# Performance work log

Hardware: AMD Instinct MI355X
Metric: run time of the kernel (lower is better)

The kernel has to match this reference:

```python
import jax, jax.numpy as jnp
import numpy as np

D_MODEL = 1024
N_HEADS = 16
HEAD_DIM = D_MODEL // N_HEADS
FFN_DIM = 4096
N_EXPERTS = 8
CAP_FRAC = 0.25          # moe_eval_capacity_token_fraction (eval mode)
MOE_TOKEN_DROPOUT = 0.2  # eval: expert output scaled by (1 - p)
LN_EPS = 1e-5
B, S = 4, 512


def setup_inputs():
    key = jax.random.key(0)
    ks = jax.random.split(key, 20)
    def w(k, shape, scale=0.02):
        return jax.random.normal(k, shape, jnp.float32) * scale
    return {
        "x": jax.random.normal(ks[0], (B, S, D_MODEL), jnp.float32),
        "wq": w(ks[1], (D_MODEL, D_MODEL)), "bq": w(ks[2], (D_MODEL,)),
        "wk": w(ks[3], (D_MODEL, D_MODEL)), "bk": w(ks[4], (D_MODEL,)),
        "wv": w(ks[5], (D_MODEL, D_MODEL)), "bv": w(ks[6], (D_MODEL,)),
        "wo": w(ks[7], (D_MODEL, D_MODEL)), "bo": w(ks[8], (D_MODEL,)),
        "ln1_g": 1.0 + w(ks[9], (D_MODEL,)), "ln1_b": w(ks[10], (D_MODEL,)),
        "ln2_g": 1.0 + w(ks[11], (D_MODEL,)), "ln2_b": w(ks[12], (D_MODEL,)),
        "wr": w(ks[13], (D_MODEL, N_EXPERTS)),
        "w1": w(ks[14], (N_EXPERTS, D_MODEL, FFN_DIM)), "b1": w(ks[15], (N_EXPERTS, FFN_DIM)),
        "w2": w(ks[16], (N_EXPERTS, FFN_DIM, D_MODEL)), "b2": w(ks[17], (N_EXPERTS, D_MODEL)),
    }


def _layer_norm(x, g, b):
    mu = x.mean(-1, keepdims=True)
    var = ((x - mu) ** 2).mean(-1, keepdims=True)
    return (x - mu) * jax.lax.rsqrt(var + LN_EPS) * g + b


def _self_attention(x, wq, bq, wk, bk, wv, bv, wo, bo):
    b, s, d = x.shape
    q = ((x @ wq + bq) * (HEAD_DIM ** -0.5)).reshape(b, s, N_HEADS, HEAD_DIM)
    k = (x @ wk + bk).reshape(b, s, N_HEADS, HEAD_DIM)
    v = (x @ wv + bv).reshape(b, s, N_HEADS, HEAD_DIM)
    scores = jnp.einsum('bqhd,bkhd->bhqk', q, k)
    p = jax.nn.softmax(scores, axis=-1)
    o = jnp.einsum('bhqk,bkhd->bqhd', p, v).reshape(b, s, d)
    return o @ wo + bo


def _moe_ffn(x, wr, w1, b1, w2, b2):
    # x: [T, D]. NLLB-MoE top-2 router with capacity dropping (eval mode,
    # second_expert_policy='all', normalize_router_prob_before_dropping=False).
    T, D = x.shape
    C = int(np.ceil(CAP_FRAC * T))  # static expert capacity
    logits = x @ wr                                    # [T, E] router dtype fp32
    probs = jax.nn.softmax(logits, axis=-1)
    top1 = jnp.argmax(probs, axis=-1)                  # [T]
    m1 = jax.nn.one_hot(top1, N_EXPERTS, dtype=x.dtype)
    top2 = jnp.argmax(jnp.where(m1 > 0, -jnp.inf, logits), axis=-1)
    m2 = jax.nn.one_hot(top2, N_EXPERTS, dtype=x.dtype)
    loc1 = jnp.cumsum(m1, axis=0) - 1.0                # slot within expert
    loc2 = jnp.cumsum(m2, axis=0) - 1.0 + m1.sum(0, keepdims=True)
    m1 = m1 * (loc1 < C)                               # capacity dropping
    m2 = m2 * (loc2 < C)
    t1 = (probs * m1).sum(-1)
    t2 = (probs * m2).sum(-1)
    denom = jnp.maximum(t1 + t2, jnp.finfo(x.dtype).eps)
    t1, t2 = t1 / denom, t2 / denom
    tok = jnp.arange(T)
    s1 = loc1[tok, top1].astype(jnp.int32)
    s2 = loc2[tok, top2].astype(jnp.int32)
    v1 = m1[tok, top1] > 0
    v2 = m2[tok, top2] > 0
    s1 = jnp.where(v1, s1, C)  # out-of-range slot -> dropped by scatter
    s2 = jnp.where(v2, s2, C)
    # dispatch tokens to capacity buffers [E, C, D] (slots are unique)
    buf = jnp.zeros((N_EXPERTS, C, D), x.dtype)
    buf = buf.at[top1, s1].set(x, mode='drop')
    buf = buf.at[top2, s2].set(x, mode='drop')
    # grouped expert FFN (relu), eval-mode moe_token_dropout scaling
    h = jax.nn.relu(jnp.einsum('ecd,edf->ecf', buf, w1) + b1[:, None, :])
    y = (jnp.einsum('ecf,efd->ecd', h, w2) + b2[:, None, :]) * (1.0 - MOE_TOKEN_DROPOUT)
    # combine with normalized top-2 gates (dropped tokens get gate 0)
    y1 = y[top1, jnp.minimum(s1, C - 1)]
    y2 = y[top2, jnp.minimum(s2, C - 1)]
    g1 = t1 * v1
    g2 = t2 * v2
    return g1[:, None] * y1 + g2[:, None] * y2


def reference(x, wq, bq, wk, bk, wv, bv, wo, bo, ln1_g, ln1_b, ln2_g, ln2_b, wr, w1, b1, w2, b2):
    # Pre-LN self-attention block
    h = _layer_norm(x, ln1_g, ln1_b)
    h = _self_attention(h, wq, bq, wk, bk, wv, bv, wo, bo)
    x = x + h
    # Pre-LN sparse MoE FFN block
    h = _layer_norm(x, ln2_g, ln2_b)
    b, s, d = h.shape
    moe = _moe_ffn(h.reshape(b * s, d), wr, w1, b1, w2, b2).reshape(b, s, d)
    return x + moe
```

## Files before the change

### kernel.cpp

```cpp
#include <hip/hip_runtime.h>
#include <hip/hip_bf16.h>
#include <stdint.h>

#define T_TOK 2048
#define DM 1024
#define NHEAD 16
#define HDIM 64
#define SEQ 512
#define NEXP 8
#define FFN 4096
#define CAP 512
#define LN_EPSV 1e-5f
#define ROUTER_EPS 1.1920929e-07f

typedef __bf16 bf16x8 __attribute__((ext_vector_type(8)));
typedef float f32x4 __attribute__((ext_vector_type(4)));

__device__ __forceinline__ void gld_lds16(const __hip_bfloat16* g, __hip_bfloat16* l) {
  __builtin_amdgcn_global_load_lds(
      (const __attribute__((address_space(1))) void*)g,
      (__attribute__((address_space(3))) void*)l, 16, 0, 0);
}

__device__ __forceinline__ void xcd_remap(int& bx, int& by, int& bz) {
  int gx = gridDim.x, gy = gridDim.y, gz = gridDim.z;
  int nwg = gx * gy * gz;
  int lin = (blockIdx.z * gy + blockIdx.y) * gx + blockIdx.x;
  int q = nwg >> 3;
  int lin2 = (lin & 7) * q + (lin >> 3);
  int gxy = gx * gy;
  bz = lin2 / gxy;
  int rem = lin2 - bz * gxy;
  by = rem / gx;
  bx = rem - by * gx;
}

__global__ void transpose_cvt(const float* __restrict__ W, __hip_bfloat16* __restrict__ WT,
                              int R, int Cc) {
  __shared__ float tile[32][33];
  int e = blockIdx.z;
  const float* src = W + (size_t)e * R * Cc;
  __hip_bfloat16* dst = WT + (size_t)e * R * Cc;
  int c0 = blockIdx.x * 32, r0 = blockIdx.y * 32;
  int tx = threadIdx.x, ty = threadIdx.y;
#pragma unroll
  for (int i = 0; i < 4; i++) {
    int r = r0 + ty + i * 8;
    tile[ty + i * 8][tx] = src[(size_t)r * Cc + c0 + tx];
  }
  __syncthreads();
#pragma unroll
  for (int i = 0; i < 4; i++) {
    int c = c0 + ty + i * 8;
    dst[(size_t)c * R + r0 + tx] = __float2bfloat16(tile[tx][ty + i * 8]);
  }
}

__global__ void transpose_cvt_hp(const float* __restrict__ W, __hip_bfloat16* __restrict__ WH,
                                 __hip_bfloat16* __restrict__ WL, int R, int Cc, float scale) {
  __shared__ float tile[32][33];
  int c0 = blockIdx.x * 32, r0 = blockIdx.y * 32;
  int tx = threadIdx.x, ty = threadIdx.y;
#pragma unroll
  for (int i = 0; i < 4; i++) {
    int r = r0 + ty + i * 8;
    tile[ty + i * 8][tx] = W[(size_t)r * Cc + c0 + tx];
  }
  __syncthreads();
#pragma unroll
  for (int i = 0; i < 4; i++) {
    int c = c0 + ty + i * 8;
    float v = tile[tx][ty + i * 8] * scale;
    __hip_bfloat16 h = __float2bfloat16(v);
    WH[(size_t)c * R + r0 + tx] = h;
    WL[(size_t)c * R + r0 + tx] = __float2bfloat16(v - __bfloat162float(h));
  }
}

__global__ __launch_bounds__(256) void pack_bias(const float* __restrict__ bq,
                                                 const float* __restrict__ bk,
                                                 const float* __restrict__ bv,
                                                 float* __restrict__ outp) {
  int t = blockIdx.x * 256 + threadIdx.x;
  if (t < DM) outp[t] = bq[t] * 0.125f;
  else if (t < 2 * DM) outp[t] = bk[t - DM];
  else if (t < 3 * DM) outp[t] = bv[t - 2 * DM];
}

__global__ __launch_bounds__(256) void ln1_hp(const float* __restrict__ x,
                                              const float* __restrict__ g,
                                              const float* __restrict__ bta,
                                              __hip_bfloat16* __restrict__ ohi,
                                              __hip_bfloat16* __restrict__ olo) {
  int row = blockIdx.x, t = threadIdx.x;
  const float4* xr = (const float4*)(x + (size_t)row * DM);
  float4 v = xr[t];
  float s = v.x + v.y + v.z + v.w;
  float ss = v.x * v.x + v.y * v.y + v.z * v.z + v.w * v.w;
  __shared__ float rs[4], rss[4];
  __shared__ float smu, sinv;
  int wid = t >> 6, lane = t & 63;
  for (int off = 32; off; off >>= 1) { s += __shfl_down(s, off); ss += __shfl_down(ss, off); }
  if (!lane) { rs[wid] = s; rss[wid] = ss; }
  __syncthreads();
  if (!t) {
    float S = rs[0] + rs[1] + rs[2] + rs[3], SS = rss[0] + rss[1] + rss[2] + rss[3];
    float mu = S / DM;
    float var = SS / DM - mu * mu;
    smu = mu; sinv = 1.0f / sqrtf(var + LN_EPSV);
  }
  __syncthreads();
  float mu = smu, inv = sinv;
  float4 gv = ((const float4*)g)[t], bv = ((const float4*)bta)[t];
  float n[4];
  n[0] = (v.x - mu) * inv * gv.x + bv.x;
  n[1] = (v.y - mu) * inv * gv.y + bv.y;
  n[2] = (v.z - mu) * inv * gv.z + bv.z;
  n[3] = (v.w - mu) * inv * gv.w + bv.w;
  __hip_bfloat16* hr = ohi + (size_t)row * DM + t * 4;
  __hip_bfloat16* lr = olo + (size_t)row * DM + t * 4;
#pragma unroll
  for (int k = 0; k < 4; k++) {
    __hip_bfloat16 h = __float2bfloat16(n[k]);
    hr[k] = h;
    lr[k] = __float2bfloat16(n[k] - __bfloat162float(h));
  }
}

__global__ __launch_bounds__(256) void cvt_hp(const float* __restrict__ in,
                                              __hip_bfloat16* __restrict__ hi,
                                              __hip_bfloat16* __restrict__ lo) {
  int i = (blockIdx.x * 256 + threadIdx.x) * 4;
  float4 v = *(const float4*)&in[i];
  float n[4] = {v.x, v.y, v.z, v.w};
#pragma unroll
  for (int k = 0; k < 4; k++) {
    __hip_bfloat16 h = __float2bfloat16(n[k]);
    hi[i + k] = h;
    lo[i + k] = __float2bfloat16(n[k] - __bfloat162float(h));
  }
}

template <int BM, int BN, int TM, int TN, bool BT>
__global__ __launch_bounds__(256) void gemm_f32(
    const float* __restrict__ A, const float* __restrict__ B, float* __restrict__ Cc,
    const float* __restrict__ bias, const float* __restrict__ resid,
    int M, int N, int K, int lda, int ldb, int ldc, float scale, int zdiv,
    long long sA1, long long sA2, long long sB1, long long sB2,
    long long sC1, long long sC2) {
  constexpr int BK = 16;
  __shared__ float As[BK][BM + 4];
  __shared__ float Bs[BK][BN + 4];
  int z = blockIdx.z;
  int zq = z / zdiv, zr = z % zdiv;
  A += zq * sA1 + zr * sA2;
  B += zq * sB1 + zr * sB2;
  Cc += zq * sC1 + zr * sC2;
  int tid = threadIdx.x;
  int m0 = blockIdx.y * BM, n0 = blockIdx.x * BN;
  constexpr int NTX = BN / TN;
  int tx = tid % NTX, ty = tid / NTX;
  float acc[TM][TN] = {};
  for (int k0 = 0; k0 < K; k0 += BK) {
    constexpr int ALOADS = BM * BK / (256 * 4);
#pragma unroll
    for (int i = 0; i < ALOADS; i++) {
      int idx = tid + i * 256;
      int m = idx / (BK / 4);
      int kk = (idx % (BK / 4)) * 4;
      float4 va = *(const float4*)&A[(size_t)(m0 + m) * lda + k0 + kk];
      As[kk + 0][m] = va.x; As[kk + 1][m] = va.y; As[kk + 2][m] = va.z; As[kk + 3][m] = va.w;
    }
    constexpr int BLOADS = BK * BN / (256 * 4);
    if (!BT) {
#pragma unroll
      for (int i = 0; i < BLOADS; i++) {
        int idx = tid + i * 256;
        int kk = idx / (BN / 4);
        int n = (idx % (BN / 4)) * 4;
        *(float4*)&Bs[kk][n] = *(const float4*)&B[(size_t)(k0 + kk) * ldb + n0 + n];
      }
    } else {
#pragma unroll
      for (int i = 0; i < BLOADS; i++) {
        int idx = tid + i * 256;
        int n = idx / (BK / 4);
        int kk = (idx % (BK / 4)) * 4;
        float4 vb = *(const float4*)&B[(size_t)(n0 + n) * ldb + k0 + kk];
        Bs[kk + 0][n] = vb.x; Bs[kk + 1][n] = vb.y; Bs[kk + 2][n] = vb.z; Bs[kk + 3][n] = vb.w;
      }
    }
    __syncthreads();
#pragma unroll
    for (int kk = 0; kk < BK; kk++) {
      float ar[TM], br[TN];
#pragma unroll
      for (int i = 0; i < TM; i += 4) *(float4*)&ar[i] = *(const float4*)&As[kk][ty * TM + i];
#pragma unroll
      for (int j = 0; j < TN; j += 4) *(float4*)&br[j] = *(const float4*)&Bs[kk][tx * TN + j];
#pragma unroll
      for (int i = 0; i < TM; i++)
#pragma unroll
        for (int j = 0; j < TN; j++) acc[i][j] += ar[i] * br[j];
    }
    __syncthreads();
  }
#pragma unroll
  for (int i = 0; i < TM; i++) {
    int m = m0 + ty * TM + i;
#pragma unroll
    for (int j = 0; j < TN; j++) {
      int n = n0 + tx * TN + j;
      float v = acc[i][j];
      if (bias) v += bias[n];
      v *= scale;
      if (resid) v += resid[(size_t)m * ldc + n];
      acc[i][j] = v;
    }
#pragma unroll
    for (int j = 0; j < TN; j += 4)
      *(float4*)&Cc[(size_t)m * ldc + n0 + tx * TN + j] = *(float4*)&acc[i][j];
  }
}

__global__ __launch_bounds__(256) void softmax_rows(float* __restrict__ sc) {
  int row = blockIdx.x, t = threadIdx.x;
  float* p = sc + (size_t)row * SEQ;
  float2 v = *(const float2*)&p[t * 2];
  float mx = fmaxf(v.x, v.y);
  __shared__ float r[4];
  __shared__ float bmax, bsum;
  int wid = t >> 6, lane = t & 63;
  for (int off = 32; off; off >>= 1) mx = fmaxf(mx, __shfl_down(mx, off));
  if (!lane) r[wid] = mx;
  __syncthreads();
  if (!t) bmax = fmaxf(fmaxf(r[0], r[1]), fmaxf(r[2], r[3]));
  __syncthreads();
  mx = bmax;
  float e0 = __expf(v.x - mx), e1v = __expf(v.y - mx);
  float s = e0 + e1v;
  for (int off = 32; off; off >>= 1) s += __shfl_down(s, off);
  if (!lane) r[wid] = s;
  __syncthreads();
  if (!t) bsum = r[0] + r[1] + r[2] + r[3];
  __syncthreads();
  float inv = 1.0f / bsum;
  float2 o; o.x = e0 * inv; o.y = e1v * inv;
  *(float2*)&p[t * 2] = o;
}

template <int MODE>
__global__ __launch_bounds__(256) void gemm_hp(
    const __hip_bfloat16* __restrict__ Ahi, const __hip_bfloat16* __restrict__ Alo,
    const __hip_bfloat16* __restrict__ Bhi, const __hip_bfloat16* __restrict__ Blo,
    float* __restrict__ Cc, const float* __restrict__ bias, const float* __restrict__ resid,
    int M, int N, int K, long long sB, long long sC, int biasStride) {
  constexpr int BM = 128, BN = 128, BK = 32;
  __shared__ __align__(16) __hip_bfloat16 AsH[2][BM * BK];
  __shared__ __align__(16) __hip_bfloat16 AsL[2][BM * BK];
  __shared__ __align__(16) __hip_bfloat16 BsH[2][BN * BK];
  __shared__ __align__(16) __hip_bfloat16 BsL[2][BN * BK];
  int bx, by, bz;
  xcd_remap(bx, by, bz);
  int e = bz;
  Bhi += (size_t)e * sB; Blo += (size_t)e * sB;
  size_t czoff = (size_t)e * sC;
  const float* bvec = bias + (size_t)e * biasStride;
  int m0 = by * BM, n0 = bx * BN;
  int tid = threadIdx.x;
  int lane = tid & 63, quad = lane >> 4, l16 = lane & 15, wv = tid >> 6;
  int wm = wv >> 1, wn = wv & 1;
  f32x4 acc[4][4] = {};
  auto STAGE = [&](int buf, int k0) {
#pragma unroll
    for (int i = 0; i < 2; i++) {
      int flat = tid + i * 256;
      int r = flat >> 2, lc = flat & 3;
      int pc = lc ^ ((r >> 1) & 3);
      gld_lds16(Ahi + (size_t)(m0 + r) * K + k0 + pc * 8, &AsH[buf][flat * 8]);
      gld_lds16(Alo + (size_t)(m0 + r) * K + k0 + pc * 8, &AsL[buf][flat * 8]);
      gld_lds16(Bhi + (size_t)(n0 + r) * K + k0 + pc * 8, &BsH[buf][flat * 8]);
      gld_lds16(Blo + (size_t)(n0 + r) * K + k0 + pc * 8, &BsL[buf][flat * 8]);
    }
  };
  STAGE(0, 0);
  __syncthreads();
  int KT = K / BK;
  for (int kt = 0; kt < KT; kt++) {
    int cur = kt & 1;
    if (kt + 1 < KT) STAGE(cur ^ 1, (kt + 1) * BK);
    bf16x8 ah[4], al[4], bh[4], bl[4];
#pragma unroll
    for (int i = 0; i < 4; i++) {
      int r = wm * 64 + i * 16 + l16;
      int pc = quad ^ ((r >> 1) & 3);
      ah[i] = *(const bf16x8*)(&AsH[cur][r * BK + pc * 8]);
      al[i] = *(const bf16x8*)(&AsL[cur][r * BK + pc * 8]);
    }
#pragma unroll
    for (int j = 0; j < 4; j++) {
      int r = wn * 64 + j * 16 + l16;
      int pc = quad ^ ((r >> 1) & 3);
      bh[j] = *(const bf16x8*)(&BsH[cur][r * BK + pc * 8]);
      bl[j] = *(const bf16x8*)(&BsL[cur][r * BK + pc * 8]);
    }
#pragma unroll
    for (int i = 0; i < 4; i++)
#pragma unroll
      for (int j = 0; j < 4; j++) {
        acc[i][j] = __builtin_amdgcn_mfma_f32_16x16x32_bf16(ah[i], bh[j], acc[i][j], 0, 0, 0);
        acc[i][j] = __builtin_amdgcn_mfma_f32_16x16x32_bf16(ah[i], bl[j], acc[i][j], 0, 0, 0);
        acc[i][j] = __builtin_amdgcn_mfma_f32_16x16x32_bf16(al[i], bh[j], acc[i][j], 0, 0, 0);
      }
    __syncthreads();
  }
#pragma unroll
  for (int j = 0; j < 4; j++) {
    int col = n0 + wn * 64 + j * 16 + l16;
    float bb = bvec[col];
#pragma unroll
    for (int i = 0; i < 4; i++) {
      int row0 = m0 + wm * 64 + i * 16 + quad * 4;
#pragma unroll
      for (int r = 0; r < 4; r++) {
        float v = acc[i][j][r] + bb;
        if (MODE == 3) v += resid[(size_t)(row0 + r) * N + col];
        Cc[czoff + (size_t)(row0 + r) * N + col] = v;
      }
    }
  }
}

__global__ __launch_bounds__(256) void ln2_router(const float* __restrict__ x2,
                                                  const float* __restrict__ g,
                                                  const float* __restrict__ bta,
                                                  const float* __restrict__ wr,
                                                  __hip_bfloat16* __restrict__ h2,
                                                  float* __restrict__ logits) {
  int row = blockIdx.x, t = threadIdx.x;
  const float4* xr = (const float4*)(x2 + (size_t)row * DM);
  float4 v = xr[t];
  float s = v.x + v.y + v.z + v.w;
  float ss = v.x * v.x + v.y * v.y + v.z * v.z + v.w * v.w;
  __shared__ float rs[4], rss[4];
  __shared__ float smu, sinv;
  int wid = t >> 6, lane = t & 63;
  for (int off = 32; off; off >>= 1) { s += __shfl_down(s, off); ss += __shfl_down(ss, off); }
  if (!lane) { rs[wid] = s; rss[wid] = ss; }
  __syncthreads();
  if (!t) {
    float S = rs[0] + rs[1] + rs[2] + rs[3], SS = rss[0] + rss[1] + rss[2] + rss[3];
    float mu = S / DM;
    float var = SS / DM - mu * mu;
    smu = mu; sinv = 1.0f / sqrtf(var + LN_EPSV);
  }
  __syncthreads();
  float mu = smu, inv = sinv;
  float4 gv = ((const float4*)g)[t], bv = ((const float4*)bta)[t];
  float n0 = (v.x - mu) * inv * gv.x + bv.x;
  float n1 = (v.y - mu) * inv * gv.y + bv.y;
  float n2 = (v.z - mu) * inv * gv.z + bv.z;
  float n3 = (v.w - mu) * inv * gv.w + bv.w;
  __hip_bfloat16* hr = h2 + (size_t)row * DM + t * 4;
  hr[0] = __float2bfloat16(n0); hr[1] = __float2bfloat16(n1);
  hr[2] = __float2bfloat16(n2); hr[3] = __float2bfloat16(n3);
  const float* w0 = wr + (size_t)(t * 4) * NEXP;
  __shared__ float red[256 * NEXP];
#pragma unroll
  for (int e = 0; e < NEXP; e++)
    red[t * NEXP + e] = n0 * w0[e] + n1 * w0[NEXP + e] + n2 * w0[2 * NEXP + e] + n3 * w0[3 * NEXP + e];
  __syncthreads();
  for (int sdt = 128; sdt > 0; sdt >>= 1) {
    if (t < sdt) {
#pragma unroll
      for (int e = 0; e < NEXP; e++) red[t * NEXP + e] += red[(t + sdt) * NEXP + e];
    }
    __syncthreads();
  }
  if (t < NEXP) logits[(size_t)row * NEXP + t] = red[t];
}

__global__ __launch_bounds__(256) void routing(const float* __restrict__ logits,
                                               int* __restrict__ e1o, int* __restrict__ s1o,
                                               float* __restrict__ g1o,
                                               int* __restrict__ e2o, int* __restrict__ s2o,
                                               float* __restrict__ g2o,
                                               int* __restrict__ src_tok) {
  __shared__ unsigned char t1s[T_TOK], t2s[T_TOK];
  __shared__ unsigned short r1s[T_TOK], r2s[T_TOK];
  __shared__ int cnt1s[NEXP];
  int t = threadIdx.x;
  for (int i = t; i < NEXP * CAP; i += 256) src_tok[i] = -1;
  for (int tok = t; tok < T_TOK; tok += 256) {
    float lg[NEXP];
#pragma unroll
    for (int e = 0; e < NEXP; e++) lg[e] = logits[(size_t)tok * NEXP + e];
    int b1 = 0; float m1v = lg[0];
#pragma unroll
    for (int e = 1; e < NEXP; e++) if (lg[e] > m1v) { m1v = lg[e]; b1 = e; }
    int b2 = -1; float m2v = -3.4e38f;
#pragma unroll
    for (int e = 0; e < NEXP; e++) if (e != b1 && lg[e] > m2v) { m2v = lg[e]; b2 = e; }
    t1s[tok] = (unsigned char)b1; t2s[tok] = (unsigned char)b2;
  }
  __syncthreads();
  if (t < 64) {
    int base[NEXP] = {0, 0, 0, 0, 0, 0, 0, 0};
    for (int c = 0; c < T_TOK / 64; c++) {
      int tok = c * 64 + t;
      int my = t1s[tok];
      unsigned long long below = (1ull << t) - 1ull;
#pragma unroll
      for (int e = 0; e < NEXP; e++) {
        unsigned long long msk = __ballot(my == e);
        if (my == e) r1s[tok] = (unsigned short)(base[e] + __popcll(msk & below));
        base[e] += (int)__popcll(msk);
      }
    }
    if (t == 0) {
#pragma unroll
      for (int e = 0; e < NEXP; e++) cnt1s[e] = base[e];
    }
#pragma unroll
    for (int e = 0; e < NEXP; e++) base[e] = 0;
    for (int c = 0; c < T_TOK / 64; c++) {
      int tok = c * 64 + t;
      int my = t2s[tok];
      unsigned long long below = (1ull << t) - 1ull;
#pragma unroll
      for (int e = 0; e < NEXP; e++) {
        unsigned long long msk = __ballot(my == e);
        if (my == e) r2s[tok] = (unsigned short)(base[e] + __popcll(msk & below));
        base[e] += (int)__popcll(msk);
      }
    }
  }
  __syncthreads();
  for (int tok = t; tok < T_TOK; tok += 256) {
    float lg[NEXP];
#pragma unroll
    for (int e = 0; e < NEXP; e++) lg[e] = logits[(size_t)tok * NEXP + e];
    int b1 = t1s[tok], b2 = t2s[tok];
    float lb1 = lg[0], lb2 = lg[0];
#pragma unroll
    for (int e = 0; e < NEXP; e++) { if (e == b1) lb1 = lg[e]; if (e == b2) lb2 = lg[e]; }
    float sum = 0.f;
#pragma unroll
    for (int e = 0; e < NEXP; e++) sum += __expf(lg[e] - lb1);
    float p1 = 1.0f / sum;
    float p2 = __expf(lb2 - lb1) / sum;
    int sl1 = r1s[tok];
    int sl2 = r2s[tok] + cnt1s[b2];
    bool v1 = sl1 < CAP, v2 = sl2 < CAP;
    float tt1 = v1 ? p1 : 0.f, tt2 = v2 ? p2 : 0.f;
    float den = fmaxf(tt1 + tt2, ROUTER_EPS);
    float gg1 = v1 ? tt1 / den : 0.f;
    float gg2 = v2 ? tt2 / den : 0.f;
    e1o[tok] = b1; s1o[tok] = v1 ? sl1 : 0; g1o[tok] = gg1;
    e2o[tok] = b2; s2o[tok] = v2 ? sl2 : 0; g2o[tok] = gg2;
    if (v1) src_tok[b1 * CAP + sl1] = tok;
    if (v2) src_tok[b2 * CAP + sl2] = tok;
  }
}

__global__ __launch_bounds__(64) void dispatch(const int* __restrict__ src_tok,
                                               const __hip_bfloat16* __restrict__ h2,
                                               __hip_bfloat16* __restrict__ Amoe) {
  int rowb = blockIdx.x, t = threadIdx.x;
  int tok = src_tok[rowb];
  uint4* dst = (uint4*)(Amoe + (size_t)rowb * DM);
  if (tok >= 0) {
    const uint4* src = (const uint4*)(h2 + (size_t)tok * DM);
    dst[t] = src[t]; dst[t + 64] = src[t + 64];
  } else {
    uint4 z = make_uint4(0, 0, 0, 0);
    dst[t] = z; dst[t + 64] = z;
  }
}

template <int MODE>
__global__ __launch_bounds__(256) void gemm_bf16(
    const __hip_bfloat16* __restrict__ A, const __hip_bfloat16* __restrict__ Bt,
    __hip_bfloat16* __restrict__ Cc, const float* __restrict__ bias,
    int M, int N, int K, long long sA, long long sB, long long sC, int biasStride) {
  constexpr int BM = 128, BN = 128, BK = 64;
  __shared__ __align__(16) __hip_bfloat16 Asm[2][BM * BK];
  __shared__ __align__(16) __hip_bfloat16 Bsm[2][BN * BK];
  int bx, by, bz;
  xcd_remap(bx, by, bz);
  int e = bz;
  A += (size_t)e * sA; Bt += (size_t)e * sB; Cc += (size_t)e * sC;
  const float* bvec = bias + (size_t)e * biasStride;
  int m0 = by * BM, n0 = bx * BN;
  int tid = threadIdx.x;
  int lane = tid & 63, quad = lane >> 4, l16 = lane & 15, wv = tid >> 6;
  int wm = wv >> 1, wn = wv & 1;
  f32x4 acc[4][4] = {};
  auto STAGE = [&](int buf, int k0) {
#pragma unroll
    for (int i = 0; i < 4; i++) {
      int flat = tid + i * 256;
      int r = flat >> 3, lc = flat & 7;
      int pc = lc ^ (r & 7);
      gld_lds16(A + (size_t)(m0 + r) * K + k0 + pc * 8, &Asm[buf][flat * 8]);
      gld_lds16(Bt + (size_t)(n0 + r) * K + k0 + pc * 8, &Bsm[buf][flat * 8]);
    }
  };
  STAGE(0, 0);
  __syncthreads();
  int KT = K / BK;
  for (int kt = 0; kt < KT; kt++) {
    int cur = kt & 1;
    if (kt + 1 < KT) STAGE(cur ^ 1, (kt + 1) * BK);
#pragma unroll
    for (int ks = 0; ks < 2; ks++) {
      bf16x8 af[4], bfr[4];
#pragma unroll
      for (int i = 0; i < 4; i++) {
        int r = wm * 64 + i * 16 + l16;
        int pc = (ks * 4 + quad) ^ (r & 7);
        af[i] = *(const bf16x8*)(&Asm[cur][r * BK + pc * 8]);
      }
#pragma unroll
      for (int j = 0; j < 4; j++) {
        int r = wn * 64 + j * 16 + l16;
        int pc = (ks * 4 + quad) ^ (r & 7);
        bfr[j] = *(const bf16x8*)(&Bsm[cur][r * BK + pc * 8]);
      }
#pragma unroll
      for (int i = 0; i < 4; i++)
#pragma unroll
        for (int j = 0; j < 4; j++)
          acc[i][j] = __builtin_amdgcn_mfma_f32_16x16x32_bf16(af[i], bfr[j], acc[i][j], 0, 0, 0);
    }
    __syncthreads();
  }
#pragma unroll
  for (int j = 0; j < 4; j++) {
    int col = n0 + wn * 64 + j * 16 + l16;
    float bb = bvec[col];
#pragma unroll
    for (int i = 0; i < 4; i++) {
      int row0 = m0 + wm * 64 + i * 16 + quad * 4;
#pragma unroll
      for (int r = 0; r < 4; r++) {
        float v = acc[i][j][r] + bb;
        if (MODE == 0) v = fmaxf(v, 0.0f);
        else v *= 0.8f;
        Cc[(size_t)(row0 + r) * N + col] = __float2bfloat16(v);
      }
    }
  }
}

__global__ __launch_bounds__(64) void combine(const float* __restrict__ x2,
                                              const __hip_bfloat16* __restrict__ Y,
                                              const int* __restrict__ e1, const int* __restrict__ s1,
                                              const float* __restrict__ g1,
                                              const int* __restrict__ e2, const int* __restrict__ s2,
                                              const float* __restrict__ g2,
                                              float* __restrict__ out) {
  int tok = blockIdx.x, t = threadIdx.x;
  float gg1 = g1[tok], gg2 = g2[tok];
  const __hip_bfloat16* y1 = Y + ((size_t)e1[tok] * CAP + s1[tok]) * DM;
  const __hip_bfloat16* y2 = Y + ((size_t)e2[tok] * CAP + s2[tok]) * DM;
  const float* xr = x2 + (size_t)tok * DM;
  float* orow = out + (size_t)tok * DM;
#pragma unroll
  for (int j = 0; j < 4; j++) {
    int idx = t * 4 + j * 256;
    float4 vv = *(const float4*)&xr[idx];
    float4 r;
    r.x = vv.x + gg1 * __bfloat162float(y1[idx + 0]) + gg2 * __bfloat162float(y2[idx + 0]);
    r.y = vv.y + gg1 * __bfloat162float(y1[idx + 1]) + gg2 * __bfloat162float(y2[idx + 1]);
    r.z = vv.z + gg1 * __bfloat162float(y1[idx + 2]) + gg2 * __bfloat162float(y2[idx + 2]);
    r.w = vv.w + gg1 * __bfloat162float(y1[idx + 3]) + gg2 * __bfloat162float(y2[idx + 3]);
    *(float4*)&orow[idx] = r;
  }
}

extern "C" void kernel_launch(void* const* d_in, const int* in_sizes, int n_in,
                              void* d_out, int out_size, void* d_ws, size_t ws_size,
                              hipStream_t stream) {
  (void)in_sizes; (void)n_in; (void)out_size; (void)ws_size;
  const float* x    = (const float*)d_in[0];
  const float* wq   = (const float*)d_in[1];
  const float* bq   = (const float*)d_in[2];
  const float* wk   = (const float*)d_in[3];
  const float* bk   = (const float*)d_in[4];
  const float* wv   = (const float*)d_in[5];
  const float* bv   = (const float*)d_in[6];
  const float* wo   = (const float*)d_in[7];
  const float* bo   = (const float*)d_in[8];
  const float* ln1g = (const float*)d_in[9];
  const float* ln1b = (const float*)d_in[10];
  const float* ln2g = (const float*)d_in[11];
  const float* ln2b = (const float*)d_in[12];
  const float* wr   = (const float*)d_in[13];
  const float* w1   = (const float*)d_in[14];
  const float* b1   = (const float*)d_in[15];
  const float* w2   = (const float*)d_in[16];
  const float* b2   = (const float*)d_in[17];
  float* out = (float*)d_out;
  char* ws = (char*)d_ws;

  __hip_bfloat16* W1T  = (__hip_bfloat16*)(ws + 0);
  __hip_bfloat16* W2T  = (__hip_bfloat16*)(ws + 67108864);
  float* sc            = (float*)(ws + 134217728);
  __hip_bfloat16* h1hi = (__hip_bfloat16*)(ws + 134217728);
  __hip_bfloat16* h1lo = (__hip_bfloat16*)(ws + 138412032);
  float* bqkv          = (float*)(ws + 142606336);
  __hip_bfloat16* WQKVH= (__hip_bfloat16*)(ws + 143654912);
  __hip_bfloat16* WQKVL= (__hip_bfloat16*)(ws + 149946368);
  __hip_bfloat16* Hm   = (__hip_bfloat16*)(ws + 134217728);
  float* logits        = (float*)(ws + 167772160);
  int*   e1a           = (int*)(ws + 167837696);
  int*   s1a           = (int*)(ws + 167845888);
  int*   e2a           = (int*)(ws + 167854080);
  int*   s2a           = (int*)(ws + 167862272);
  float* g1a           = (float*)(ws + 167870464);
  float* g2a           = (float*)(ws + 167878656);
  int*   src_tok       = (int*)(ws + 167886848);
  float* qkv           = (float*)(ws + 201326592);
  float* q             = qkv;
  float* k_            = qkv + 2097152;
  float* v             = qkv + 4194304;
  float* o_f           = (float*)(ws + 201326592);
  float* x2            = (float*)(ws + 201326592);
  __hip_bfloat16* ohi  = (__hip_bfloat16*)(ws + 209715200);
  __hip_bfloat16* olo  = (__hip_bfloat16*)(ws + 213909504);
  __hip_bfloat16* Y    = (__hip_bfloat16*)(ws + 209715200);
  __hip_bfloat16* h2   = (__hip_bfloat16*)(ws + 218103808);
  __hip_bfloat16* Amoe = (__hip_bfloat16*)(ws + 222298112);
  __hip_bfloat16* WOH  = (__hip_bfloat16*)(ws + 226492416);
  __hip_bfloat16* WOL  = (__hip_bfloat16*)(ws + 228589568);

  transpose_cvt<<<dim3(FFN / 32, DM / 32, NEXP), dim3(32, 8), 0, stream>>>(w1, W1T, DM, FFN);
  transpose_cvt<<<dim3(DM / 32, FFN / 32, NEXP), dim3(32, 8), 0, stream>>>(w2, W2T, FFN, DM);
  transpose_cvt_hp<<<dim3(DM / 32, DM / 32, 1), dim3(32, 8), 0, stream>>>(
      wq, WQKVH, WQKVL, DM, DM, 0.125f);
  transpose_cvt_hp<<<dim3(DM / 32, DM / 32, 1), dim3(32, 8), 0, stream>>>(
      wk, WQKVH + (size_t)DM * DM, WQKVL + (size_t)DM * DM, DM, DM, 1.0f);
  transpose_cvt_hp<<<dim3(DM / 32, DM / 32, 1), dim3(32, 8), 0, stream>>>(
      wv, WQKVH + (size_t)2 * DM * DM, WQKVL + (size_t)2 * DM * DM, DM, DM, 1.0f);
  transpose_cvt_hp<<<dim3(DM / 32, DM / 32, 1), dim3(32, 8), 0, stream>>>(
      wo, WOH, WOL, DM, DM, 1.0f);
  pack_bias<<<3 * DM / 256, 256, 0, stream>>>(bq, bk, bv, bqkv);
  ln1_hp<<<T_TOK, 256, 0, stream>>>(x, ln1g, ln1b, h1hi, h1lo);
  gemm_hp<2><<<dim3(DM / 128, T_TOK / 128, 3), 256, 0, stream>>>(
      h1hi, h1lo, WQKVH, WQKVL, qkv, bqkv, nullptr, T_TOK, DM, DM,
      (long long)DM * DM, (long long)T_TOK * DM, DM);
  gemm_f32<128, 128, 8, 8, true><<<dim3(SEQ / 128, SEQ / 128, 64), 256, 0, stream>>>(
      q, k_, sc, nullptr, nullptr, SEQ, SEQ, HDIM, DM, DM, SEQ, 1.0f, NHEAD,
      (long long)SEQ * DM, HDIM, (long long)SEQ * DM, HDIM,
      (long long)NHEAD * SEQ * SEQ, (long long)SEQ * SEQ);
  softmax_rows<<<64 * SEQ, 256, 0, stream>>>(sc);
  gemm_f32<128, 64, 8, 4, false><<<dim3(1, SEQ / 128, 64), 256, 0, stream>>>(
      sc, v, o_f, nullptr, nullptr, SEQ, HDIM, SEQ, SEQ, DM, DM, 1.0f, NHEAD,
      (long long)NHEAD * SEQ * SEQ, (long long)SEQ * SEQ,
      (long long)SEQ * DM, HDIM, (long long)SEQ * DM, HDIM);
  cvt_hp<<<T_TOK * DM / 1024, 256, 0, stream>>>(o_f, ohi, olo);
  gemm_hp<3><<<dim3(DM / 128, T_TOK / 128, 1), 256, 0, stream>>>(
      ohi, olo, WOH, WOL, x2, bo, x, T_TOK, DM, DM, 0LL, 0LL, 0);
  ln2_router<<<T_TOK, 256, 0, stream>>>(x2, ln2g, ln2b, wr, h2, logits);
  routing<<<1, 256, 0, stream>>>(logits, e1a, s1a, g1a, e2a, s2a, g2a, src_tok);
  dispatch<<<NEXP * CAP, 64, 0, stream>>>(src_tok, h2, Amoe);
  gemm_bf16<0><<<dim3(FFN / 128, CAP / 128, NEXP), 256, 0, stream>>>(
      Amoe, W1T, Hm, b1, CAP, FFN, DM,
      (long long)CAP * DM, (long long)FFN * DM, (long long)CAP * FFN, FFN);
  gemm_bf16<1><<<dim3(DM / 128, CAP / 128, NEXP), 256, 0, stream>>>(
      Hm, W2T, Y, b2, CAP, DM, FFN,
      (long long)CAP * FFN, (long long)DM * FFN, (long long)CAP * DM, DM);
  combine<<<T_TOK, 64, 0, stream>>>(x2, Y, e1a, s1a, g1a, e2a, s2a, g2a, out);
}
```

Baseline: 760.9 us.

## Templatize GEMM tiles, reorder prefetch after LDS reads, add single-buffer path

Makes the tile shapes and warp layout of the hi/lo split and bf16 GEMM kernels template parameters. The QKV, output-projection and second expert GEMMs now use smaller tiles, giving more blocks for better CU fill. The next-tile global-to-LDS prefetch is moved to after the fragment reads, behind a sched_barrier. The first expert GEMM uses a new single-buffered path to halve LDS use and raise occupancy, at the cost of exposing load latency on each k step.

```diff
diff --git a/kernel.cpp b/kernel.cpp
--- a/kernel.cpp
+++ b/kernel.cpp
@@ -249,13 +249,14 @@
   *(float2*)&p[t * 2] = o;
 }
 
-template <int MODE>
+template <int MODE, int BM, int BN, int WM, int WN>
 __global__ __launch_bounds__(256) void gemm_hp(
     const __hip_bfloat16* __restrict__ Ahi, const __hip_bfloat16* __restrict__ Alo,
     const __hip_bfloat16* __restrict__ Bhi, const __hip_bfloat16* __restrict__ Blo,
     float* __restrict__ Cc, const float* __restrict__ bias, const float* __restrict__ resid,
     int M, int N, int K, long long sB, long long sC, int biasStride) {
-  constexpr int BM = 128, BN = 128, BK = 32;
+  constexpr int BK = 32;
+  constexpr int MI = BM / WM / 16, NJ = BN / WN / 16;
   __shared__ __align__(16) __hip_bfloat16 AsH[2][BM * BK];
   __shared__ __align__(16) __hip_bfloat16 AsL[2][BM * BK];
   __shared__ __align__(16) __hip_bfloat16 BsH[2][BN * BK];
@@ -269,16 +270,24 @@
   int m0 = by * BM, n0 = bx * BN;
   int tid = threadIdx.x;
   int lane = tid & 63, quad = lane >> 4, l16 = lane & 15, wv = tid >> 6;
-  int wm = wv >> 1, wn = wv & 1;
-  f32x4 acc[4][4] = {};
+  int wm = wv / WN, wn = wv % WN;
+  f32x4 acc[MI][NJ] = {};
   auto STAGE = [&](int buf, int k0) {
-#pragma unroll
-    for (int i = 0; i < 2; i++) {
+    constexpr int ACH = BM * (BK / 8) / 256;
+#pragma unroll
+    for (int i = 0; i < ACH; i++) {
       int flat = tid + i * 256;
       int r = flat >> 2, lc = flat & 3;
       int pc = lc ^ ((r >> 1) & 3);
       gld_lds16(Ahi + (size_t)(m0 + r) * K + k0 + pc * 8, &AsH[buf][flat * 8]);
       gld_lds16(Alo + (size_t)(m0 + r) * K + k0 + pc * 8, &AsL[buf][flat * 8]);
+    }
+    constexpr int BCH = BN * (BK / 8) / 256;
+#pragma unroll
+    for (int i = 0; i < BCH; i++) {
+      int flat = tid + i * 256;
+      int r = flat >> 2, lc = flat & 3;
+      int pc = lc ^ ((r >> 1) & 3);
       gld_lds16(Bhi + (size_t)(n0 + r) * K + k0 + pc * 8, &BsH[buf][flat * 8]);
       gld_lds16(Blo + (size_t)(n0 + r) * K + k0 + pc * 8, &BsL[buf][flat * 8]);
     }
@@ -288,26 +297,27 @@
   int KT = K / BK;
   for (int kt = 0; kt < KT; kt++) {
     int cur = kt & 1;
-    if (kt + 1 < KT) STAGE(cur ^ 1, (kt + 1) * BK);
-    bf16x8 ah[4], al[4], bh[4], bl[4];
-#pragma unroll
-    for (int i = 0; i < 4; i++) {
-      int r = wm * 64 + i * 16 + l16;
+    bf16x8 ah[MI], al[MI], bh[NJ], bl[NJ];
+#pragma unroll
+    for (int i = 0; i < MI; i++) {
+      int r = wm * (BM / WM) + i * 16 + l16;
       int pc = quad ^ ((r >> 1) & 3);
       ah[i] = *(const bf16x8*)(&AsH[cur][r * BK + pc * 8]);
       al[i] = *(const bf16x8*)(&AsL[cur][r * BK + pc * 8]);
     }
 #pragma unroll
-    for (int j = 0; j < 4; j++) {
-      int r = wn * 64 + j * 16 + l16;
+    for (int j = 0; j < NJ; j++) {
+      int r = wn * (BN / WN) + j * 16 + l16;
       int pc = quad ^ ((r >> 1) & 3);
       bh[j] = *(const bf16x8*)(&BsH[cur][r * BK + pc * 8]);
       bl[j] = *(const bf16x8*)(&BsL[cur][r * BK + pc * 8]);
     }
-#pragma unroll
-    for (int i = 0; i < 4; i++)
-#pragma unroll
-      for (int j = 0; j < 4; j++) {
+    __builtin_amdgcn_sched_barrier(0);
+    if (kt + 1 < KT) STAGE(cur ^ 1, (kt + 1) * BK);
+#pragma unroll
+    for (int i = 0; i < MI; i++)
+#pragma unroll
+      for (int j = 0; j < NJ; j++) {
         acc[i][j] = __builtin_amdgcn_mfma_f32_16x16x32_bf16(ah[i], bh[j], acc[i][j], 0, 0, 0);
         acc[i][j] = __builtin_amdgcn_mfma_f32_16x16x32_bf16(ah[i], bl[j], acc[i][j], 0, 0, 0);
         acc[i][j] = __builtin_amdgcn_mfma_f32_16x16x32_bf16(al[i], bh[j], acc[i][j], 0, 0, 0);
@@ -315,12 +325,12 @@
     __syncthreads();
   }
 #pragma unroll
-  for (int j = 0; j < 4; j++) {
-    int col = n0 + wn * 64 + j * 16 + l16;
+  for (int j = 0; j < NJ; j++) {
+    int col = n0 + wn * (BN / WN) + j * 16 + l16;
     float bb = bvec[col];
 #pragma unroll
-    for (int i = 0; i < 4; i++) {
-      int row0 = m0 + wm * 64 + i * 16 + quad * 4;
+    for (int i = 0; i < MI; i++) {
+      int row0 = m0 + wm * (BM / WM) + i * 16 + quad * 4;
 #pragma unroll
       for (int r = 0; r < 4; r++) {
         float v = acc[i][j][r] + bb;
@@ -478,14 +488,16 @@
   }
 }
 
-template <int MODE>
+template <int MODE, int BM, int BN, int WM, int WN, int DB>
 __global__ __launch_bounds__(256) void gemm_bf16(
     const __hip_bfloat16* __restrict__ A, const __hip_bfloat16* __restrict__ Bt,
     __hip_bfloat16* __restrict__ Cc, const float* __restrict__ bias,
     int M, int N, int K, long long sA, long long sB, long long sC, int biasStride) {
-  constexpr int BM = 128, BN = 128, BK = 64;
-  __shared__ __align__(16) __hip_bfloat16 Asm[2][BM * BK];
-  __shared__ __align__(16) __hip_bfloat16 Bsm[2][BN * BK];
+  constexpr int BK = 64;
+  constexpr int NB = DB ? 2 : 1;
+  constexpr int MI = BM / WM / 16, NJ = BN / WN / 16;
+  __shared__ __align__(16) __hip_bfloat16 Asm[NB][BM * BK];
+  __shared__ __align__(16) __hip_bfloat16 Bsm[NB][BN * BK];
   int bx, by, bz;
   xcd_remap(bx, by, bz);
   int e = bz;
@@ -494,54 +506,94 @@
   int m0 = by * BM, n0 = bx * BN;
   int tid = threadIdx.x;
   int lane = tid & 63, quad = lane >> 4, l16 = lane & 15, wv = tid >> 6;
-  int wm = wv >> 1, wn = wv & 1;
-  f32x4 acc[4][4] = {};
+  int wm = wv / WN, wn = wv % WN;
+  f32x4 acc[MI][NJ] = {};
   auto STAGE = [&](int buf, int k0) {
-#pragma unroll
-    for (int i = 0; i < 4; i++) {
+    constexpr int ACH = BM * (BK / 8) / 256;
+#pragma unroll
+    for (int i = 0; i < ACH; i++) {
       int flat = tid + i * 256;
       int r = flat >> 3, lc = flat & 7;
       int pc = lc ^ (r & 7);
       gld_lds16(A + (size_t)(m0 + r) * K + k0 + pc * 8, &Asm[buf][flat * 8]);
+    }
+    constexpr int BCH = BN * (BK / 8) / 256;
+#pragma unroll
+    for (int i = 0; i < BCH; i++) {
+      int flat = tid + i * 256;
+      int r = flat >> 3, lc = flat & 7;
+      int pc = lc ^ (r & 7);
       gld_lds16(Bt + (size_t)(n0 + r) * K + k0 + pc * 8, &Bsm[buf][flat * 8]);
     }
   };
-  STAGE(0, 0);
-  __syncthreads();
   int KT = K / BK;
-  for (int kt = 0; kt < KT; kt++) {
-    int cur = kt & 1;
-    if (kt + 1 < KT) STAGE(cur ^ 1, (kt + 1) * BK);
-#pragma unroll
-    for (int ks = 0; ks < 2; ks++) {
-      bf16x8 af[4], bfr[4];
-#pragma unroll
-      for (int i = 0; i < 4; i++) {
-        int r = wm * 64 + i * 16 + l16;
-        int pc = (ks * 4 + quad) ^ (r & 7);
-        af[i] = *(const bf16x8*)(&Asm[cur][r * BK + pc * 8]);
-      }
-#pragma unroll
-      for (int j = 0; j < 4; j++) {
-        int r = wn * 64 + j * 16 + l16;
-        int pc = (ks * 4 + quad) ^ (r & 7);
-        bfr[j] = *(const bf16x8*)(&Bsm[cur][r * BK + pc * 8]);
-      }
-#pragma unroll
-      for (int i = 0; i < 4; i++)
-#pragma unroll
-        for (int j = 0; j < 4; j++)
-          acc[i][j] = __builtin_amdgcn_mfma_f32_16x16x32_bf16(af[i], bfr[j], acc[i][j], 0, 0, 0);
-    }
+  if (DB) {
+    STAGE(0, 0);
     __syncthreads();
-  }
-#pragma unroll
-  for (int j = 0; j < 4; j++) {
-    int col = n0 + wn * 64 + j * 16 + l16;
+    for (int kt = 0; kt < KT; kt++) {
+      int cur = kt & 1;
+      bf16x8 af[2][MI], bfr[2][NJ];
+#pragma unroll
+      for (int ks = 0; ks < 2; ks++) {
+#pragma unroll
+        for (int i = 0; i < MI; i++) {
+          int r = wm * (BM / WM) + i * 16 + l16;
+          int pc = (ks * 4 + quad) ^ (r & 7);
+          af[ks][i] = *(const bf16x8*)(&Asm[cur][r * BK + pc * 8]);
+        }
+#pragma unroll
+        for (int j = 0; j < NJ; j++) {
+          int r = wn * (BN / WN) + j * 16 + l16;
+          int pc = (ks * 4 + quad) ^ (r & 7);
+          bfr[ks][j] = *(const bf16x8*)(&Bsm[cur][r * BK + pc * 8]);
+        }
+      }
+      __builtin_amdgcn_sched_barrier(0);
+      if (kt + 1 < KT) STAGE(cur ^ 1, (kt + 1) * BK);
+#pragma unroll
+      for (int ks = 0; ks < 2; ks++)
+#pragma unroll
+        for (int i = 0; i < MI; i++)
+#pragma unroll
+          for (int j = 0; j < NJ; j++)
+            acc[i][j] = __builtin_amdgcn_mfma_f32_16x16x32_bf16(af[ks][i], bfr[ks][j], acc[i][j], 0, 0, 0);
+      __syncthreads();
+    }
+  } else {
+    for (int kt = 0; kt < KT; kt++) {
+      if (kt) __syncthreads();
+      STAGE(0, kt * BK);
+      __syncthreads();
+#pragma unroll
+      for (int ks = 0; ks < 2; ks++) {
+        bf16x8 af[MI], bfr[NJ];
+#pragma unroll
+        for (int i = 0; i < MI; i++) {
+          int r = wm * (BM / WM) + i * 16 + l16;
+          int pc = (ks * 4 + quad) ^ (r & 7);
+          af[i] = *(const bf16x8*)(&Asm[0][r * BK + pc * 8]);
+        }
+#pragma unroll
+        for (int j = 0; j < NJ; j++) {
+          int r = wn * (BN / WN) + j * 16 + l16;
+          int pc = (ks * 4 + quad) ^ (r & 7);
+          bfr[j] = *(const bf16x8*)(&Bsm[0][r * BK + pc * 8]);
+        }
+#pragma unroll
+        for (int i = 0; i < MI; i++)
+#pragma unroll
+          for (int j = 0; j < NJ; j++)
+            acc[i][j] = __builtin_amdgcn_mfma_f32_16x16x32_bf16(af[i], bfr[j], acc[i][j], 0, 0, 0);
+      }
+    }
+  }
+#pragma unroll
+  for (int j = 0; j < NJ; j++) {
+    int col = n0 + wn * (BN / WN) + j * 16 + l16;
     float bb = bvec[col];
 #pragma unroll
-    for (int i = 0; i < 4; i++) {
-      int row0 = m0 + wm * 64 + i * 16 + quad * 4;
+    for (int i = 0; i < MI; i++) {
+      int row0 = m0 + wm * (BM / WM) + i * 16 + quad * 4;
 #pragma unroll
       for (int r = 0; r < 4; r++) {
         float v = acc[i][j][r] + bb;
@@ -647,7 +699,7 @@
       wo, WOH, WOL, DM, DM, 1.0f);
   pack_bias<<<3 * DM / 256, 256, 0, stream>>>(bq, bk, bv, bqkv);
   ln1_hp<<<T_TOK, 256, 0, stream>>>(x, ln1g, ln1b, h1hi, h1lo);
-  gemm_hp<2><<<dim3(DM / 128, T_TOK / 128, 3), 256, 0, stream>>>(
+  gemm_hp<2, 128, 64, 2, 2><<<dim3(DM / 64, T_TOK / 128, 3), 256, 0, stream>>>(
       h1hi, h1lo, WQKVH, WQKVL, qkv, bqkv, nullptr, T_TOK, DM, DM,
       (long long)DM * DM, (long long)T_TOK * DM, DM);
   gemm_f32<128, 128, 8, 8, true><<<dim3(SEQ / 128, SEQ / 128, 64), 256, 0, stream>>>(
@@ -660,15 +712,15 @@
       (long long)NHEAD * SEQ * SEQ, (long long)SEQ * SEQ,
       (long long)SEQ * DM, HDIM, (long long)SEQ * DM, HDIM);
   cvt_hp<<<T_TOK * DM / 1024, 256, 0, stream>>>(o_f, ohi, olo);
-  gemm_hp<3><<<dim3(DM / 128, T_TOK / 128, 1), 256, 0, stream>>>(
+  gemm_hp<3, 64, 64, 2, 2><<<dim3(DM / 64, T_TOK / 64, 1), 256, 0, stream>>>(
       ohi, olo, WOH, WOL, x2, bo, x, T_TOK, DM, DM, 0LL, 0LL, 0);
   ln2_router<<<T_TOK, 256, 0, stream>>>(x2, ln2g, ln2b, wr, h2, logits);
   routing<<<1, 256, 0, stream>>>(logits, e1a, s1a, g1a, e2a, s2a, g2a, src_tok);
   dispatch<<<NEXP * CAP, 64, 0, stream>>>(src_tok, h2, Amoe);
-  gemm_bf16<0><<<dim3(FFN / 128, CAP / 128, NEXP), 256, 0, stream>>>(
+  gemm_bf16<0, 128, 128, 2, 2, 0><<<dim3(FFN / 128, CAP / 128, NEXP), 256, 0, stream>>>(
       Amoe, W1T, Hm, b1, CAP, FFN, DM,
       (long long)CAP * DM, (long long)FFN * DM, (long long)CAP * FFN, FFN);
-  gemm_bf16<1><<<dim3(DM / 128, CAP / 128, NEXP), 256, 0, stream>>>(
+  gemm_bf16<1, 128, 64, 2, 2, 1><<<dim3(DM / 64, CAP / 128, NEXP), 256, 0, stream>>>(
       Hm, W2T, Y, b2, CAP, DM, FFN,
       (long long)CAP * FFN, (long long)DM * FFN, (long long)CAP * DM, DM);
   combine<<<T_TOK, 64, 0, stream>>>(x2, Y, e1a, s1a, g1a, e2a, s2a, g2a, out);
```

Result: faster. 719.4 us (-5.5%).
